# Kernel tuning notes

Measured on AMD Instinct MI355X. Metric: run time of the kernel, lower is better.

## Reference

```python
import jax, jax.numpy as jnp
import numpy as np

NEG_BIG = -9.0e15  # matches torch zero_vec constant


def setup_inputs() -> dict:
    key = jax.random.key(0)
    k1, k2, k3, k4, k5 = jax.random.split(key, 5)
    B, N, D_IN, D_HID, D_OUT = 4, 4096, 128, 64, 128
    h = jax.random.normal(k1, (B, N, D_IN), dtype=jnp.float32)
    adj = jax.random.randint(k2, (N, N), 0, 2, dtype=jnp.int32)
    Ws = jax.random.normal(k3, (D_IN, D_HID), dtype=jnp.float32) * (1.414 / np.sqrt(D_IN))
    Wt = jax.random.normal(k4, (D_IN, D_HID), dtype=jnp.float32) * (1.414 / np.sqrt(D_IN))
    Wc = jax.random.normal(k5, (D_IN, D_OUT), dtype=jnp.float32) * np.sqrt(2.0 / D_IN)
    return {"h": h, "adj": adj, "Ws": Ws, "Wt": Wt, "Wc": Wc}


def reference(h, adj, Ws, Wt, Wc):
    # h: [B,N,D_in], adj: [N,N] broadcast over batch
    Whs = jnp.matmul(h, Ws)                     # [B,N,H]
    Wht = jnp.matmul(h, Wt)                     # [B,N,H]
    e = jnp.einsum('bnh,bmh->bnm', Whs, Wht)    # [B,N,N] dense scores
    z = jnp.where(adj > 0, e, NEG_BIG)          # adjacency mask
    alpha = jax.nn.softmax(z, axis=-1)          # [B,N,N]
    Whc = jnp.matmul(h, Wc)                     # [B,N,D_out]
    h_prime = jnp.matmul(alpha, Whc)            # [B,N,D_out]
    return h_prime
```

## Files before the change

### kernel.cpp

```cpp
#include <hip/hip_runtime.h>
#include <hip/hip_bf16.h>

#define NTOK 4096
#define BATCH 4
#define DIN 128
#define DHID 64
#define DOUT 128
#define NWRD (NTOK / 32)
#define SPLIT 4
#define ITERS (NTOK / SPLIT / 64)
#define NEG_BIG -9.0e15f
#define LOG2E 1.44269504088896340736f

typedef short short8 __attribute__((ext_vector_type(8)));
typedef float floatx4 __attribute__((ext_vector_type(4)));

static __device__ __forceinline__ unsigned short f2bf(float f) {
    unsigned int u = __builtin_bit_cast(unsigned int, f);
    u = (u + 0x7fffu + ((u >> 16) & 1u)) >> 16;
    return (unsigned short)u;
}
static __device__ __forceinline__ float bf2f(unsigned short s) {
    unsigned int u = ((unsigned int)s) << 16;
    return __builtin_bit_cast(float, u);
}
static __device__ __forceinline__ unsigned int pk2(float lo, float hi) {
    unsigned int r;
    asm("v_cvt_pk_bf16_f32 %0, %1, %2" : "=v"(r) : "v"(lo), "v"(hi));
    return r;
}
static __device__ __forceinline__ float ex2(float x) {
    float r;
    asm("v_exp_f32 %0, %1" : "=v"(r) : "v"(x));
    return r;
}

static __device__ __forceinline__ floatx4 mfma16(short8 a, short8 b, floatx4 c) {
    return __builtin_amdgcn_mfma_f32_16x16x32_bf16(a, b, c, 0, 0, 0);
}

__global__ __launch_bounds__(256) void pack_adj_kernel(const int* __restrict__ adj,
                                                       unsigned int* __restrict__ bits) {
    int w = blockIdx.x * 256 + threadIdx.x;
    const int4* p = reinterpret_cast<const int4*>(adj) + (size_t)w * 8;
    unsigned int m = 0;
#pragma unroll
    for (int i = 0; i < 8; ++i) {
        int4 v = p[i];
        m |= (v.x > 0 ? 1u : 0u) << (4 * i + 0);
        m |= (v.y > 0 ? 1u : 0u) << (4 * i + 1);
        m |= (v.z > 0 ? 1u : 0u) << (4 * i + 2);
        m |= (v.w > 0 ? 1u : 0u) << (4 * i + 3);
    }
    bits[w] = m;
}

__global__ __launch_bounds__(256) void conv_w_kernel(const float* __restrict__ Ws,
                                                     const float* __restrict__ Wt,
                                                     const float* __restrict__ Wc,
                                                     unsigned short* __restrict__ WT_hi,
                                                     unsigned short* __restrict__ WT_lo) {
    int idx = blockIdx.x * 256 + threadIdx.x;
    int k = idx >> 8, col = idx & 255;
    float w;
    if (col < 64) w = Ws[k * DHID + col] * LOG2E;
    else if (col < 128) w = Wt[k * DHID + (col - 64)];
    else w = Wc[k * DOUT + (col - 128)];
    unsigned short hi = f2bf(w);
    WT_hi[col * DIN + k] = hi;
    if (col < 128) WT_lo[col * DIN + k] = f2bf(w - bf2f(hi));
}

__global__ __launch_bounds__(256) void prep_kernel(const float* __restrict__ h,
                                                   const unsigned short* __restrict__ WT_hi,
                                                   const unsigned short* __restrict__ WT_lo,
                                                   unsigned short* __restrict__ Whs_hi,
                                                   unsigned short* __restrict__ Whs_lo,
                                                   unsigned short* __restrict__ Wht_hi,
                                                   unsigned short* __restrict__ Wht_lo,
                                                   unsigned short* __restrict__ WhcT) {
    int tid = threadIdx.x;
    int b = blockIdx.y;
    int w = tid >> 6, lane = tid & 63, lg = lane >> 4, lc = lane & 15;
    int n0 = blockIdx.x * 16;
    const float* hrow = h + (size_t)(b * NTOK + n0 + lc) * DIN;

    short8 ah[4], al[4];
#pragma unroll
    for (int ks = 0; ks < 4; ++ks) {
        float4 f0 = *reinterpret_cast<const float4*>(hrow + ks * 32 + lg * 8);
        float4 f1 = *reinterpret_cast<const float4*>(hrow + ks * 32 + lg * 8 + 4);
        float x[8] = {f0.x, f0.y, f0.z, f0.w, f1.x, f1.y, f1.z, f1.w};
        short8 hh, ll;
#pragma unroll
        for (int j = 0; j < 8; ++j) {
            unsigned short hb = f2bf(x[j]);
            hh[j] = (short)hb;
            ll[j] = (short)f2bf(x[j] - bf2f(hb));
        }
        ah[ks] = hh;
        al[ks] = ll;
    }

#pragma unroll
    for (int ci = 0; ci < 4; ++ci) {
        int ct = w * 4 + ci;
        int col = ct * 16 + lc;
        const unsigned short* bbase = WT_hi + (size_t)col * DIN;
        const unsigned short* lbase = WT_lo + (size_t)col * DIN;
        floatx4 acc = {0.f, 0.f, 0.f, 0.f};
#pragma unroll
        for (int ks = 0; ks < 4; ++ks) {
            short8 bh = *reinterpret_cast<const short8*>(bbase + ks * 32 + lg * 8);
            acc = mfma16(ah[ks], bh, acc);
            if (w < 2) {
                short8 bl = *reinterpret_cast<const short8*>(lbase + ks * 32 + lg * 8);
                acc = mfma16(ah[ks], bl, acc);
                acc = mfma16(al[ks], bh, acc);
            }
        }
        int nr = n0 + 4 * lg;
        if (w == 0) {
#pragma unroll
            for (int r = 0; r < 4; ++r) {
                float v = acc[r];
                unsigned short hb = f2bf(v);
                size_t o = (size_t)(b * NTOK + nr + r) * DHID + col;
                Whs_hi[o] = hb;
                Whs_lo[o] = f2bf(v - bf2f(hb));
            }
        } else if (w == 1) {
#pragma unroll
            for (int r = 0; r < 4; ++r) {
                float v = acc[r];
                unsigned short hb = f2bf(v);
                size_t o = (size_t)(b * NTOK + nr + r) * DHID + (col - 64);
                Wht_hi[o] = hb;
                Wht_lo[o] = f2bf(v - bf2f(hb));
            }
        } else {
            int pcol = (nr & ~31) | ((nr & 8) << 1) | ((nr & 4) << 1) | ((nr & 16) >> 2);
            unsigned int p01 = (unsigned int)f2bf(acc[0]) | ((unsigned int)f2bf(acc[1]) << 16);
            unsigned int p23 = (unsigned int)f2bf(acc[2]) | ((unsigned int)f2bf(acc[3]) << 16);
            unsigned int* dst =
                reinterpret_cast<unsigned int*>(&WhcT[(size_t)(b * DOUT + col - 128) * NTOK + pcol]);
            dst[0] = p01;
            dst[1] = p23;
        }
    }
}

__global__ __launch_bounds__(256, 2) void attn_kernel(const unsigned short* __restrict__ Whs_hi,
                                                      const unsigned short* __restrict__ Whs_lo,
                                                      const unsigned short* __restrict__ Wht_hi,
                                                      const unsigned short* __restrict__ Wht_lo,
                                                      const unsigned short* __restrict__ WhcT,
                                                      const unsigned int* __restrict__ bits,
                                                      unsigned short* __restrict__ po,
                                                      float* __restrict__ pm,
                                                      float* __restrict__ pl) {
    __shared__ unsigned short Kh_lds[64][72];
    __shared__ unsigned short Kl_lds[64][72];
    __shared__ unsigned short V_lds[128][72];

    int tid = threadIdx.x;
    int b = blockIdx.y;
    int split = blockIdx.z;
    int kbase = split * (ITERS * 64);
    int lane = tid & 63, lg = lane >> 4, lc = lane & 15;
    int q0 = blockIdx.x * 128 + (tid >> 6) * 32;
    int nA = q0 + lc, nB = q0 + 16 + lc;

    const unsigned short* qAH = Whs_hi + (size_t)(b * NTOK + nA) * DHID;
    const unsigned short* qAL = Whs_lo + (size_t)(b * NTOK + nA) * DHID;
    const unsigned short* qBH = Whs_hi + (size_t)(b * NTOK + nB) * DHID;
    const unsigned short* qBL = Whs_lo + (size_t)(b * NTOK + nB) * DHID;
    short8 qAh0 = *reinterpret_cast<const short8*>(qAH + lg * 8);
    short8 qAh1 = *reinterpret_cast<const short8*>(qAH + 32 + lg * 8);
    short8 qAl0 = *reinterpret_cast<const short8*>(qAL + lg * 8);
    short8 qAl1 = *reinterpret_cast<const short8*>(qAL + 32 + lg * 8);
    short8 qBh0 = *reinterpret_cast<const short8*>(qBH + lg * 8);
    short8 qBh1 = *reinterpret_cast<const short8*>(qBH + 32 + lg * 8);
    short8 qBl0 = *reinterpret_cast<const short8*>(qBL + lg * 8);
    short8 qBl1 = *reinterpret_cast<const short8*>(qBL + 32 + lg * 8);

    floatx4 o0[8], o1[8];
#pragma unroll
    for (int dt = 0; dt < 8; ++dt) {
        o0[dt] = (floatx4){0.f, 0.f, 0.f, 0.f};
        o1[dt] = (floatx4){0.f, 0.f, 0.f, 0.f};
    }
    float mA = NEG_BIG, lA = 0.f, mB = NEG_BIG, lB = 0.f;

    int kkey = tid >> 2, koff = (tid & 3) * 16;
    int vd = tid >> 1, va = tid & 1;

    short8 krH0, krH1, krL0, krL1, vr0, vr1, vr2, vr3;
    unsigned int mwA0, mwA1, mwB0, mwB1;

    {
        int kb = kbase;
        const unsigned short* ksrcH = Wht_hi + (size_t)(b * NTOK + kb + kkey) * DHID + koff;
        const unsigned short* ksrcL = Wht_lo + (size_t)(b * NTOK + kb + kkey) * DHID + koff;
        krH0 = *reinterpret_cast<const short8*>(ksrcH);
        krH1 = *reinterpret_cast<const short8*>(ksrcH + 8);
        krL0 = *reinterpret_cast<const short8*>(ksrcL);
        krL1 = *reinterpret_cast<const short8*>(ksrcL + 8);
        const unsigned short* vsrc = WhcT + (size_t)(b * DOUT + vd) * NTOK + kb + va * 32;
        vr0 = *reinterpret_cast<const short8*>(vsrc);
        vr1 = *reinterpret_cast<const short8*>(vsrc + 8);
        vr2 = *reinterpret_cast<const short8*>(vsrc + 16);
        vr3 = *reinterpret_cast<const short8*>(vsrc + 24);
        mwA0 = bits[nA * NWRD + (kb >> 5)];
        mwA1 = bits[nA * NWRD + (kb >> 5) + 1];
        mwB0 = bits[nB * NWRD + (kb >> 5)];
        mwB1 = bits[nB * NWRD + (kb >> 5) + 1];
    }

    for (int it = 0; it < ITERS; ++it) {
        __syncthreads();
        *reinterpret_cast<short8*>(&Kh_lds[kkey][koff]) = krH0;
        *reinterpret_cast<short8*>(&Kh_lds[kkey][koff + 8]) = krH1;
        *reinterpret_cast<short8*>(&Kl_lds[kkey][koff]) = krL0;
        *reinterpret_cast<short8*>(&Kl_lds[kkey][koff + 8]) = krL1;
        *reinterpret_cast<short8*>(&V_lds[vd][va * 32]) = vr0;
        *reinterpret_cast<short8*>(&V_lds[vd][va * 32 + 8]) = vr1;
        *reinterpret_cast<short8*>(&V_lds[vd][va * 32 + 16]) = vr2;
        *reinterpret_cast<short8*>(&V_lds[vd][va * 32 + 24]) = vr3;
        __syncthreads();

        floatx4 s0[4], s1[4];
        __builtin_amdgcn_s_setprio(1);
#pragma unroll
        for (int kc = 0; kc < 4; ++kc) {
            short8 kh0 = *reinterpret_cast<const short8*>(&Kh_lds[kc * 16 + lc][lg * 8]);
            short8 kh1 = *reinterpret_cast<const short8*>(&Kh_lds[kc * 16 + lc][32 + lg * 8]);
            short8 kl0 = *reinterpret_cast<const short8*>(&Kl_lds[kc * 16 + lc][lg * 8]);
            short8 kl1 = *reinterpret_cast<const short8*>(&Kl_lds[kc * 16 + lc][32 + lg * 8]);
            floatx4 a0 = {0.f, 0.f, 0.f, 0.f};
            a0 = mfma16(kh0, qAh0, a0);
            a0 = mfma16(kh1, qAh1, a0);
            a0 = mfma16(kh0, qAl0, a0);
            a0 = mfma16(kh1, qAl1, a0);
            a0 = mfma16(kl0, qAh0, a0);
            a0 = mfma16(kl1, qAh1, a0);
            s0[kc] = a0;
            floatx4 a1 = {0.f, 0.f, 0.f, 0.f};
            a1 = mfma16(kh0, qBh0, a1);
            a1 = mfma16(kh1, qBh1, a1);
            a1 = mfma16(kh0, qBl0, a1);
            a1 = mfma16(kh1, qBl1, a1);
            a1 = mfma16(kl0, qBh0, a1);
            a1 = mfma16(kl1, qBh1, a1);
            s1[kc] = a1;
        }
        __builtin_amdgcn_s_setprio(0);

#pragma unroll
        for (int kc = 0; kc < 4; ++kc) {
            unsigned int wA = (kc & 2) ? mwA1 : mwA0;
            unsigned int wB = (kc & 2) ? mwB1 : mwB0;
#pragma unroll
            for (int r = 0; r < 4; ++r) {
                int bit = 16 * (kc & 1) + 4 * lg + r;
                if (!((wA >> bit) & 1u)) s0[kc][r] = NEG_BIG;
                if (!((wB >> bit) & 1u)) s1[kc][r] = NEG_BIG;
            }
        }

        if (it + 1 < ITERS) {
            int kb = kbase + (it + 1) * 64;
            const unsigned short* ksrcH = Wht_hi + (size_t)(b * NTOK + kb + kkey) * DHID + koff;
            const unsigned short* ksrcL = Wht_lo + (size_t)(b * NTOK + kb + kkey) * DHID + koff;
            krH0 = *reinterpret_cast<const short8*>(ksrcH);
            krH1 = *reinterpret_cast<const short8*>(ksrcH + 8);
            krL0 = *reinterpret_cast<const short8*>(ksrcL);
            krL1 = *reinterpret_cast<const short8*>(ksrcL + 8);
            const unsigned short* vsrc = WhcT + (size_t)(b * DOUT + vd) * NTOK + kb + va * 32;
            vr0 = *reinterpret_cast<const short8*>(vsrc);
            vr1 = *reinterpret_cast<const short8*>(vsrc + 8);
            vr2 = *reinterpret_cast<const short8*>(vsrc + 16);
            vr3 = *reinterpret_cast<const short8*>(vsrc + 24);
            mwA0 = bits[nA * NWRD + (kb >> 5)];
            mwA1 = bits[nA * NWRD + (kb >> 5) + 1];
            mwB0 = bits[nB * NWRD + (kb >> 5)];
            mwB1 = bits[nB * NWRD + (kb >> 5) + 1];
        }

        {
            float vm = s0[0][0];
#pragma unroll
            for (int kc = 0; kc < 4; ++kc)
#pragma unroll
                for (int r = 0; r < 4; ++r) vm = fmaxf(vm, s0[kc][r]);
            vm = fmaxf(vm, __shfl_xor(vm, 16));
            vm = fmaxf(vm, __shfl_xor(vm, 32));
            bool skip = __all(vm <= mA + 4.0f);
            float mn = skip ? mA : fmaxf(mA, vm);
            float rs = 0.f;
#pragma unroll
            for (int kc = 0; kc < 4; ++kc)
#pragma unroll
                for (int r = 0; r < 4; ++r) {
                    float p = ex2(s0[kc][r] - mn);
                    s0[kc][r] = p;
                    rs += p;
                }
            rs += __shfl_xor(rs, 16);
            rs += __shfl_xor(rs, 32);
            if (!skip) {
                float sc = ex2(mA - mn);
                lA = lA * sc + rs;
                mA = mn;
                float sc4[4];
#pragma unroll
                for (int r = 0; r < 4; ++r) sc4[r] = __shfl(sc, (lane & 48) + 4 * lg + r);
#pragma unroll
                for (int dt = 0; dt < 8; ++dt)
#pragma unroll
                    for (int r = 0; r < 4; ++r) o0[dt][r] *= sc4[r];
            } else {
                lA += rs;
            }
        }
        {
            float vm = s1[0][0];
#pragma unroll
            for (int kc = 0; kc < 4; ++kc)
#pragma unroll
                for (int r = 0; r < 4; ++r) vm = fmaxf(vm, s1[kc][r]);
            vm = fmaxf(vm, __shfl_xor(vm, 16));
            vm = fmaxf(vm, __shfl_xor(vm, 32));
            bool skip = __all(vm <= mB + 4.0f);
            float mn = skip ? mB : fmaxf(mB, vm);
            float rs = 0.f;
#pragma unroll
            for (int kc = 0; kc < 4; ++kc)
#pragma unroll
                for (int r = 0; r < 4; ++r) {
                    float p = ex2(s1[kc][r] - mn);
                    s1[kc][r] = p;
                    rs += p;
                }
            rs += __shfl_xor(rs, 16);
            rs += __shfl_xor(rs, 32);
            if (!skip) {
                float sc = ex2(mB - mn);
                lB = lB * sc + rs;
                mB = mn;
                float sc4[4];
#pragma unroll
                for (int r = 0; r < 4; ++r) sc4[r] = __shfl(sc, (lane & 48) + 4 * lg + r);
#pragma unroll
                for (int dt = 0; dt < 8; ++dt)
#pragma unroll
                    for (int r = 0; r < 4; ++r) o1[dt][r] *= sc4[r];
            } else {
                lB += rs;
            }
        }

        unsigned int pw[8];
        pw[0] = pk2(s0[0][0], s0[0][1]); pw[1] = pk2(s0[0][2], s0[0][3]);
        pw[2] = pk2(s0[1][0], s0[1][1]); pw[3] = pk2(s0[1][2], s0[1][3]);
        pw[4] = pk2(s0[2][0], s0[2][1]); pw[5] = pk2(s0[2][2], s0[2][3]);
        pw[6] = pk2(s0[3][0], s0[3][1]); pw[7] = pk2(s0[3][2], s0[3][3]);
        short8 paA0 = __builtin_bit_cast(short8, *reinterpret_cast<uint4*>(&pw[0]));
        short8 paA1 = __builtin_bit_cast(short8, *reinterpret_cast<uint4*>(&pw[4]));
        pw[0] = pk2(s1[0][0], s1[0][1]); pw[1] = pk2(s1[0][2], s1[0][3]);
        pw[2] = pk2(s1[1][0], s1[1][1]); pw[3] = pk2(s1[1][2], s1[1][3]);
        pw[4] = pk2(s1[2][0], s1[2][1]); pw[5] = pk2(s1[2][2], s1[2][3]);
        pw[6] = pk2(s1[3][0], s1[3][1]); pw[7] = pk2(s1[3][2], s1[3][3]);
        short8 paB0 = __builtin_bit_cast(short8, *reinterpret_cast<uint4*>(&pw[0]));
        short8 paB1 = __builtin_bit_cast(short8, *reinterpret_cast<uint4*>(&pw[4]));

        __builtin_amdgcn_s_setprio(1);
#pragma unroll
        for (int dt = 0; dt < 8; ++dt) {
            short8 vf0 = *reinterpret_cast<const short8*>(&V_lds[dt * 16 + lc][lg * 8]);
            o0[dt] = mfma16(paA0, vf0, o0[dt]);
            o1[dt] = mfma16(paB0, vf0, o1[dt]);
        }
#pragma unroll
        for (int dt = 0; dt < 8; ++dt) {
            short8 vf1 = *reinterpret_cast<const short8*>(&V_lds[dt * 16 + lc][32 + lg * 8]);
            o0[dt] = mfma16(paA1, vf1, o0[dt]);
            o1[dt] = mfma16(paB1, vf1, o1[dt]);
        }
        __builtin_amdgcn_s_setprio(0);
    }

    {
        float m4[4], l4[4];
#pragma unroll
        for (int r = 0; r < 4; ++r) {
            int src = (lane & 48) + 4 * lg + r;
            m4[r] = __shfl(mA, src);
            l4[r] = __shfl(lA, src);
        }
#pragma unroll
        for (int r = 0; r < 4; ++r) {
            size_t row = (size_t)(split * BATCH + b) * NTOK + q0 + 4 * lg + r;
            unsigned short* prow = po + row * DOUT;
#pragma unroll
            for (int dt = 0; dt < 8; ++dt) prow[dt * 16 + lc] = f2bf(o0[dt][r]);
            if (lc == 0) {
                pm[row] = m4[r];
                pl[row] = l4[r];
            }
        }
#pragma unroll
        for (int r = 0; r < 4; ++r) {
            int src = (lane & 48) + 4 * lg + r;
            m4[r] = __shfl(mB, src);
            l4[r] = __shfl(lB, src);
        }
#pragma unroll
        for (int r = 0; r < 4; ++r) {
            size_t row = (size_t)(split * BATCH + b) * NTOK + q0 + 16 + 4 * lg + r;
            unsigned short* prow = po + row * DOUT;
#pragma unroll
            for (int dt = 0; dt < 8; ++dt) prow[dt * 16 + lc] = f2bf(o1[dt][r]);
            if (lc == 0) {
                pm[row] = m4[r];
                pl[row] = l4[r];
            }
        }
    }
}

__global__ __launch_bounds__(256) void merge_kernel(const unsigned short* __restrict__ po,
                                                    const float* __restrict__ pm,
                                                    const float* __restrict__ pl,
                                                    float* __restrict__ out) {
    int idx = blockIdx.x * 256 + threadIdx.x;
    int d = idx & (DOUT - 1);
    size_t bn = (size_t)(idx >> 7);
    const size_t BN = (size_t)BATCH * NTOK;

    float ms[SPLIT];
#pragma unroll
    for (int s = 0; s < SPLIT; ++s) ms[s] = pm[s * BN + bn];
    float M = ms[0];
#pragma unroll
    for (int s = 1; s < SPLIT; ++s) M = fmaxf(M, ms[s]);
    float L = 0.f, acc = 0.f;
#pragma unroll
    for (int s = 0; s < SPLIT; ++s) {
        float e = ex2(ms[s] - M);
        L += pl[s * BN + bn] * e;
        acc += bf2f(po[(s * BN + bn) * DOUT + d]) * e;
    }
    out[idx] = acc / L;
}

extern "C" void kernel_launch(void* const* d_in, const int* in_sizes, int n_in,
                              void* d_out, int out_size, void* d_ws, size_t ws_size,
                              hipStream_t stream) {
    const float* h   = (const float*)d_in[0];
    const int*   adj = (const int*)d_in[1];
    const float* Ws  = (const float*)d_in[2];
    const float* Wt  = (const float*)d_in[3];
    const float* Wc  = (const float*)d_in[4];
    float* out = (float*)d_out;

    size_t nq = (size_t)BATCH * NTOK * DHID;
    unsigned short* Whs_hi = (unsigned short*)d_ws;
    unsigned short* Whs_lo = Whs_hi + nq;
    unsigned short* Wht_hi = Whs_lo + nq;
    unsigned short* Wht_lo = Wht_hi + nq;
    unsigned short* WhcT   = Wht_lo + nq;
    unsigned int*   bits   = (unsigned int*)(WhcT + (size_t)BATCH * DOUT * NTOK);
    unsigned short* WT_hi  = (unsigned short*)(bits + (size_t)NTOK * NWRD);
    unsigned short* WT_lo  = WT_hi + 256 * DIN;
    unsigned short* po     = WT_lo + 128 * DIN;
    float*          pm     = (float*)(po + (size_t)SPLIT * BATCH * NTOK * DOUT);
    float*          pl     = pm + (size_t)SPLIT * BATCH * NTOK;

    pack_adj_kernel<<<dim3(NTOK * NWRD / 256), dim3(256), 0, stream>>>(adj, bits);
    conv_w_kernel<<<dim3(128), dim3(256), 0, stream>>>(Ws, Wt, Wc, WT_hi, WT_lo);
    prep_kernel<<<dim3(NTOK / 16, BATCH), dim3(256), 0, stream>>>(
        h, WT_hi, WT_lo, Whs_hi, Whs_lo, Wht_hi, Wht_lo, WhcT);
    attn_kernel<<<dim3(NTOK / 128, BATCH, SPLIT), dim3(256), 0, stream>>>(
        Whs_hi, Whs_lo, Wht_hi, Wht_lo, WhcT, bits, po, pm, pl);
    merge_kernel<<<dim3(BATCH * NTOK * DOUT / 256), dim3(256), 0, stream>>>(po, pm, pl, out);
}
```

Baseline: 189.9 us.

## Double-buffer V via direct global-to-LDS loads and rebalance key splits to six

The V tile (WhcT) now goes straight from global memory into a double-buffered, XOR-swizzled LDS array using global_load_lds. The next tile is prefetched while the current one is consumed, and no V registers are needed. The key range is split six ways with uneven 11/10-iteration chunks, and the occupancy hint rises to 3 blocks per CU so more blocks can be resident. The intent is better overlap of memory with MFMA work and better CU fill. The cost is a larger LDS footprint, more partial outputs for the merge kernel, and register pressure under the tighter launch bound.

```diff
diff --git a/kernel.cpp b/kernel.cpp
--- a/kernel.cpp
+++ b/kernel.cpp
@@ -7,8 +7,7 @@
 #define DHID 64
 #define DOUT 128
 #define NWRD (NTOK / 32)
-#define SPLIT 4
-#define ITERS (NTOK / SPLIT / 64)
+#define NSPLIT 6
 #define NEG_BIG -9.0e15f
 #define LOG2E 1.44269504088896340736f
 
@@ -33,6 +32,11 @@
     float r;
     asm("v_exp_f32 %0, %1" : "=v"(r) : "v"(x));
     return r;
+}
+static __device__ __forceinline__ void gload_lds16(const void* g, void* l) {
+    __builtin_amdgcn_global_load_lds(
+        (const __attribute__((address_space(1))) unsigned int*)g,
+        (__attribute__((address_space(3))) unsigned int*)l, 16, 0, 0);
 }
 
 static __device__ __forceinline__ floatx4 mfma16(short8 a, short8 b, floatx4 c) {
@@ -150,7 +154,7 @@
     }
 }
 
-__global__ __launch_bounds__(256, 2) void attn_kernel(const unsigned short* __restrict__ Whs_hi,
+__global__ __launch_bounds__(256, 3) void attn_kernel(const unsigned short* __restrict__ Whs_hi,
                                                       const unsigned short* __restrict__ Whs_lo,
                                                       const unsigned short* __restrict__ Wht_hi,
                                                       const unsigned short* __restrict__ Wht_lo,
@@ -161,14 +165,16 @@
                                                       float* __restrict__ pl) {
     __shared__ unsigned short Kh_lds[64][72];
     __shared__ unsigned short Kl_lds[64][72];
-    __shared__ unsigned short V_lds[128][72];
+    __shared__ unsigned short V_lds[2][128][64];
 
     int tid = threadIdx.x;
     int b = blockIdx.y;
     int split = blockIdx.z;
-    int kbase = split * (ITERS * 64);
+    int iters = (split < 4) ? 11 : 10;
+    int kbase = (split < 5) ? 704 * split : 3456;
     int lane = tid & 63, lg = lane >> 4, lc = lane & 15;
-    int q0 = blockIdx.x * 128 + (tid >> 6) * 32;
+    int wv = tid >> 6;
+    int q0 = blockIdx.x * 128 + wv * 32;
     int nA = q0 + lc, nB = q0 + 16 + lc;
 
     const unsigned short* qAH = Whs_hi + (size_t)(b * NTOK + nA) * DHID;
@@ -193,9 +199,10 @@
     float mA = NEG_BIG, lA = 0.f, mB = NEG_BIG, lB = 0.f;
 
     int kkey = tid >> 2, koff = (tid & 3) * 16;
-    int vd = tid >> 1, va = tid & 1;
-
-    short8 krH0, krH1, krL0, krL1, vr0, vr1, vr2, vr3;
+    int vrow0 = wv * 32 + (lane >> 3);
+    int vchk = (lane & 7) ^ (lane >> 3);
+
+    short8 krH0, krH1, krL0, krL1;
     unsigned int mwA0, mwA1, mwB0, mwB1;
 
     {
@@ -206,27 +213,34 @@
         krH1 = *reinterpret_cast<const short8*>(ksrcH + 8);
         krL0 = *reinterpret_cast<const short8*>(ksrcL);
         krL1 = *reinterpret_cast<const short8*>(ksrcL + 8);
-        const unsigned short* vsrc = WhcT + (size_t)(b * DOUT + vd) * NTOK + kb + va * 32;
-        vr0 = *reinterpret_cast<const short8*>(vsrc);
-        vr1 = *reinterpret_cast<const short8*>(vsrc + 8);
-        vr2 = *reinterpret_cast<const short8*>(vsrc + 16);
-        vr3 = *reinterpret_cast<const short8*>(vsrc + 24);
         mwA0 = bits[nA * NWRD + (kb >> 5)];
         mwA1 = bits[nA * NWRD + (kb >> 5) + 1];
         mwB0 = bits[nB * NWRD + (kb >> 5)];
         mwB1 = bits[nB * NWRD + (kb >> 5) + 1];
-    }
-
-    for (int it = 0; it < ITERS; ++it) {
+#pragma unroll
+        for (int i = 0; i < 4; ++i) {
+            const unsigned short* src =
+                WhcT + (size_t)(b * DOUT + vrow0 + i * 8) * NTOK + kb + vchk * 8;
+            gload_lds16(src, &V_lds[0][(wv * 4 + i) * 8][0]);
+        }
+    }
+
+    for (int it = 0; it < iters; ++it) {
+        const int cur = it & 1;
         __syncthreads();
         *reinterpret_cast<short8*>(&Kh_lds[kkey][koff]) = krH0;
         *reinterpret_cast<short8*>(&Kh_lds[kkey][koff + 8]) = krH1;
         *reinterpret_cast<short8*>(&Kl_lds[kkey][koff]) = krL0;
         *reinterpret_cast<short8*>(&Kl_lds[kkey][koff + 8]) = krL1;
-        *reinterpret_cast<short8*>(&V_lds[vd][va * 32]) = vr0;
-        *reinterpret_cast<short8*>(&V_lds[vd][va * 32 + 8]) = vr1;
-        *reinterpret_cast<short8*>(&V_lds[vd][va * 32 + 16]) = vr2;
-        *reinterpret_cast<short8*>(&V_lds[vd][va * 32 + 24]) = vr3;
+        if (it + 1 < iters) {
+            int kb = kbase + (it + 1) * 64;
+#pragma unroll
+            for (int i = 0; i < 4; ++i) {
+                const unsigned short* src =
+                    WhcT + (size_t)(b * DOUT + vrow0 + i * 8) * NTOK + kb + vchk * 8;
+                gload_lds16(src, &V_lds[cur ^ 1][(wv * 4 + i) * 8][0]);
+            }
+        }
         __syncthreads();
 
         floatx4 s0[4], s1[4];
@@ -268,7 +282,7 @@
             }
         }
 
-        if (it + 1 < ITERS) {
+        if (it + 1 < iters) {
             int kb = kbase + (it + 1) * 64;
             const unsigned short* ksrcH = Wht_hi + (size_t)(b * NTOK + kb + kkey) * DHID + koff;
             const unsigned short* ksrcL = Wht_lo + (size_t)(b * NTOK + kb + kkey) * DHID + koff;
@@ -276,11 +290,6 @@
             krH1 = *reinterpret_cast<const short8*>(ksrcH + 8);
             krL0 = *reinterpret_cast<const short8*>(ksrcL);
             krL1 = *reinterpret_cast<const short8*>(ksrcL + 8);
-            const unsigned short* vsrc = WhcT + (size_t)(b * DOUT + vd) * NTOK + kb + va * 32;
-            vr0 = *reinterpret_cast<const short8*>(vsrc);
-            vr1 = *reinterpret_cast<const short8*>(vsrc + 8);
-            vr2 = *reinterpret_cast<const short8*>(vsrc + 16);
-            vr3 = *reinterpret_cast<const short8*>(vsrc + 24);
             mwA0 = bits[nA * NWRD + (kb >> 5)];
             mwA1 = bits[nA * NWRD + (kb >> 5) + 1];
             mwB0 = bits[nB * NWRD + (kb >> 5)];
@@ -375,15 +384,17 @@
         short8 paB1 = __builtin_bit_cast(short8, *reinterpret_cast<uint4*>(&pw[4]));
 
         __builtin_amdgcn_s_setprio(1);
+        int c0 = (lg ^ (lc & 7)) * 8;
+        int c1 = ((lg ^ 4) ^ (lc & 7)) * 8;
 #pragma unroll
         for (int dt = 0; dt < 8; ++dt) {
-            short8 vf0 = *reinterpret_cast<const short8*>(&V_lds[dt * 16 + lc][lg * 8]);
+            short8 vf0 = *reinterpret_cast<const short8*>(&V_lds[cur][dt * 16 + lc][c0]);
             o0[dt] = mfma16(paA0, vf0, o0[dt]);
             o1[dt] = mfma16(paB0, vf0, o1[dt]);
         }
 #pragma unroll
         for (int dt = 0; dt < 8; ++dt) {
-            short8 vf1 = *reinterpret_cast<const short8*>(&V_lds[dt * 16 + lc][32 + lg * 8]);
+            short8 vf1 = *reinterpret_cast<const short8*>(&V_lds[cur][dt * 16 + lc][c1]);
             o0[dt] = mfma16(paA1, vf1, o0[dt]);
             o1[dt] = mfma16(paB1, vf1, o1[dt]);
         }
@@ -438,15 +449,15 @@
     size_t bn = (size_t)(idx >> 7);
     const size_t BN = (size_t)BATCH * NTOK;
 
-    float ms[SPLIT];
-#pragma unroll
-    for (int s = 0; s < SPLIT; ++s) ms[s] = pm[s * BN + bn];
+    float ms[NSPLIT];
+#pragma unroll
+    for (int s = 0; s < NSPLIT; ++s) ms[s] = pm[s * BN + bn];
     float M = ms[0];
 #pragma unroll
-    for (int s = 1; s < SPLIT; ++s) M = fmaxf(M, ms[s]);
+    for (int s = 1; s < NSPLIT; ++s) M = fmaxf(M, ms[s]);
     float L = 0.f, acc = 0.f;
 #pragma unroll
-    for (int s = 0; s < SPLIT; ++s) {
+    for (int s = 0; s < NSPLIT; ++s) {
         float e = ex2(ms[s] - M);
         L += pl[s * BN + bn] * e;
         acc += bf2f(po[(s * BN + bn) * DOUT + d]) * e;
@@ -474,14 +485,14 @@
     unsigned short* WT_hi  = (unsigned short*)(bits + (size_t)NTOK * NWRD);
     unsigned short* WT_lo  = WT_hi + 256 * DIN;
     unsigned short* po     = WT_lo + 128 * DIN;
-    float*          pm     = (float*)(po + (size_t)SPLIT * BATCH * NTOK * DOUT);
-    float*          pl     = pm + (size_t)SPLIT * BATCH * NTOK;
+    float*          pm     = (float*)(po + (size_t)NSPLIT * BATCH * NTOK * DOUT);
+    float*          pl     = pm + (size_t)NSPLIT * BATCH * NTOK;
 
     pack_adj_kernel<<<dim3(NTOK * NWRD / 256), dim3(256), 0, stream>>>(adj, bits);
     conv_w_kernel<<<dim3(128), dim3(256), 0, stream>>>(Ws, Wt, Wc, WT_hi, WT_lo);
     prep_kernel<<<dim3(NTOK / 16, BATCH), dim3(256), 0, stream>>>(
         h, WT_hi, WT_lo, Whs_hi, Whs_lo, Wht_hi, Wht_lo, WhcT);
-    attn_kernel<<<dim3(NTOK / 128, BATCH, SPLIT), dim3(256), 0, stream>>>(
+    attn_kernel<<<dim3(NTOK / 128, BATCH, NSPLIT), dim3(256), 0, stream>>>(
         Whs_hi, Whs_lo, Wht_hi, Wht_lo, WhcT, bits, po, pm, pl);
     merge_kernel<<<dim3(BATCH * NTOK * DOUT / 256), dim3(256), 0, stream>>>(po, pm, pl, out);
 }
```

After: 247.8 us. 1.3x slower.
